# Optimization experiments

Measured on AMD Instinct MI355X. Metric: run time of the kernel, lower is better.

The kernel has to match this reference:

```python
import jax, jax.numpy as jnp
import numpy as np

B, N, E, H = 4, 2048, 288, 8
D = E // H  # head_dim = 36


def setup_inputs() -> dict:
    key = jax.random.key(0)
    ks = jax.random.split(key, 8)
    s = 1.0 / np.sqrt(E)
    return {
        "query": jax.random.normal(ks[0], (B, N, E), jnp.float32),
        "key": jax.random.normal(ks[1], (B, N, E), jnp.float32),
        "value": jax.random.normal(ks[2], (B, N, E), jnp.float32),
        "Wq": jax.random.normal(ks[3], (E, E), jnp.float32) * s,
        "bq": jnp.zeros((E,), jnp.float32),
        "Wk": jax.random.normal(ks[4], (E, E), jnp.float32) * s,
        "bk": jnp.zeros((E,), jnp.float32),
        "Wv": jax.random.normal(ks[5], (E, E), jnp.float32) * s,
        "bv": jnp.zeros((E,), jnp.float32),
        "Wo": jax.random.normal(ks[6], (E, E), jnp.float32) * s,
        "bo": jnp.zeros((E,), jnp.float32),
    }


def reference(query, key, value, Wq, bq, Wk, bk, Wv, bv, Wo, bo):
    scaling = float(D) ** (-0.5)
    q = (query @ Wq + bq) * scaling            # (B, N, E), pre-scaled as in source
    k = key @ Wk + bk                          # (B, N, E)
    v = value @ Wv + bv                        # (B, N, E)
    # split heads: per-head slices along last dim == reshape to (B, N, H, D)
    qh = q.reshape(B, N, H, D)
    kh = k.reshape(B, N, H, D)
    vh = v.reshape(B, N, H, D)
    scores = jnp.einsum("bnhd,bmhd->bhnm", qh, kh)   # (B, H, N, N)
    attn = jax.nn.softmax(scores, axis=-1)
    out = jnp.einsum("bhnm,bmhd->bnhd", attn, vh)    # (B, N, H, D)
    out = out.reshape(B, N, E)                       # concat heads
    return out @ Wo + bo
```

## Files before the change

kernel.cpp:

```cpp
#include <hip/hip_runtime.h>

#define E 288
#define NSEQ 2048
#define BATCH 4
#define NH 8
#define HD 36
#define BH (BATCH * NH)
#define ROWS (BATCH * NSEQ)

typedef _Float16 half8_t __attribute__((ext_vector_type(8)));
typedef _Float16 half4_t __attribute__((ext_vector_type(4)));
typedef float f32x4 __attribute__((ext_vector_type(4)));
typedef int i32x4 __attribute__((ext_vector_type(4)));

__device__ __forceinline__ int sw64(int row, int col) {
  return (row << 6) + ((((col >> 3) ^ row) & 7) << 3) + (col & 7);
}

__device__ __forceinline__ void gld16(const _Float16* g, _Float16* l) {
  __builtin_amdgcn_global_load_lds(
      (const __attribute__((address_space(1))) void*)g,
      (__attribute__((address_space(3))) void*)l, 16, 0, 0);
}

__device__ __forceinline__ float fexp2(float x) {
  return __builtin_amdgcn_exp2f(x);
}

__global__ __launch_bounds__(256) void split_w_kernel(
    const float* __restrict__ Wq, const float* __restrict__ Wk,
    const float* __restrict__ Wv, const float* __restrict__ Wo,
    _Float16* __restrict__ whalf) {
  const int idx = blockIdx.x * 256 + threadIdx.x;
  const int m = idx / (E * E);
  const int rem = idx - m * (E * E);
  const int k = rem / E, n = rem - k * E;
  const float* W = (m == 0) ? Wq : (m == 1) ? Wk : (m == 2) ? Wv : Wo;
  whalf[(size_t)m * (E * E) + n * E + k] = (_Float16)W[rem];
}

#define PM 128
#define PN 96
#define LDA 40

struct QKVArgs {
  const float* x[3];
  const _Float16* w[3];
  const float* bias[3];
  _Float16* out[3];
};

__global__ __launch_bounds__(256, 4) void proj_qkv_kernel(QKVArgs A) {
  __shared__ __align__(16) _Float16 a_h[PM * LDA];
  __shared__ __align__(16) _Float16 w_h[PN * LDA];

  const int tid = threadIdx.x;
  const int lane = tid & 63, wv = tid >> 6;
  const int quad = lane >> 4, l15 = lane & 15;
  const int mode = blockIdx.z;
  const float* __restrict__ x = A.x[mode];
  const _Float16* __restrict__ wh = A.w[mode];
  const int row0 = blockIdx.x * PM, col0 = blockIdx.y * PN;

  f32x4 acc[2][6];
#pragma unroll
  for (int t = 0; t < 2; ++t)
#pragma unroll
    for (int nt = 0; nt < 6; ++nt) acc[t][nt] = (f32x4){0.f, 0.f, 0.f, 0.f};

  float4 apre[4];
  i32x4 wpre[2];
#pragma unroll
  for (int iu = 0; iu < 4; ++iu) {
    const int i = tid + 256 * iu, r = i >> 3, c4 = i & 7;
    apre[iu] = *(const float4*)&x[(size_t)(row0 + r) * E + c4 * 4];
  }
  {
    const int n = tid >> 2, qd = tid & 3;
    wpre[0] = *(const i32x4*)&wh[(size_t)(col0 + n) * E + qd * 8];
    if (tid < 128) {
      const int i = tid + 256, n2 = i >> 2, q2 = i & 3;
      wpre[1] = *(const i32x4*)&wh[(size_t)(col0 + n2) * E + q2 * 8];
    }
  }

  for (int kk = 0; kk < E; kk += 32) {
    __syncthreads();
#pragma unroll
    for (int iu = 0; iu < 4; ++iu) {
      const int i = tid + 256 * iu, r = i >> 3, c4 = i & 7;
      half4_t hv = {(_Float16)apre[iu].x, (_Float16)apre[iu].y,
                    (_Float16)apre[iu].z, (_Float16)apre[iu].w};
      *(half4_t*)&a_h[r * LDA + c4 * 4] = hv;
    }
    {
      const int n = tid >> 2, qd = tid & 3;
      *(i32x4*)&w_h[n * LDA + qd * 8] = wpre[0];
      if (tid < 128) {
        const int i = tid + 256, n2 = i >> 2, q2 = i & 3;
        *(i32x4*)&w_h[n2 * LDA + q2 * 8] = wpre[1];
      }
    }
    if (kk + 32 < E) {
#pragma unroll
      for (int iu = 0; iu < 4; ++iu) {
        const int i = tid + 256 * iu, r = i >> 3, c4 = i & 7;
        apre[iu] = *(const float4*)&x[(size_t)(row0 + r) * E + kk + 32 + c4 * 4];
      }
      const int n = tid >> 2, qd = tid & 3;
      wpre[0] = *(const i32x4*)&wh[(size_t)(col0 + n) * E + kk + 32 + qd * 8];
      if (tid < 128) {
        const int i = tid + 256, n2 = i >> 2, q2 = i & 3;
        wpre[1] = *(const i32x4*)&wh[(size_t)(col0 + n2) * E + kk + 32 + q2 * 8];
      }
    }
    __syncthreads();

    half8_t ah[2];
#pragma unroll
    for (int t = 0; t < 2; ++t)
      ah[t] = *(const half8_t*)&a_h[(wv * 32 + t * 16 + l15) * LDA + quad * 8];
#pragma unroll
    for (int nt = 0; nt < 6; ++nt) {
      const half8_t bh = *(const half8_t*)&w_h[(nt * 16 + l15) * LDA + quad * 8];
#pragma unroll
      for (int t = 0; t < 2; ++t)
        acc[t][nt] = __builtin_amdgcn_mfma_f32_16x16x32_f16(ah[t], bh, acc[t][nt], 0, 0, 0);
    }
  }

  const float* __restrict__ bias = A.bias[mode];
  _Float16* __restrict__ outp = A.out[mode];
  const float scale = (mode == 0) ? 0.24044917348149868f : 1.0f;
#pragma unroll
  for (int nt = 0; nt < 6; ++nt) {
    const int col = col0 + nt * 16 + l15;
    const int h = col / 36, d = col - h * 36;
    const float bc = bias[col];
#pragma unroll
    for (int t = 0; t < 2; ++t) {
#pragma unroll
      for (int r = 0; r < 4; ++r) {
        const int row = row0 + wv * 32 + t * 16 + quad * 4 + r;
        const int b = row >> 11, n = row & (NSEQ - 1);
        const int bh = b * NH + h;
        const _Float16 val = (_Float16)((acc[t][nt][r] + bc) * scale);
        if (mode == 0) {
          outp[((size_t)bh * NSEQ + n) * 64 + d] = val;
        } else {
          const int kt = n >> 6, c = n & 63;
          if (mode == 1) {
            outp[((size_t)bh * 32 + kt) * 4096 + sw64(c, d)] = val;
          } else {
            const int pc = ((c & 15) << 2) | (c >> 4);
            outp[((size_t)bh * 32 + kt) * 3072 + sw64(d, pc)] = val;
          }
        }
      }
    }
  }
}

#define QB 128
#define KT 64
#define SPLIT 4

__device__ __forceinline__ void stage_tile(const _Float16* kg, const _Float16* vg,
                                           _Float16* kb, _Float16* vb, int w,
                                           int lane) {
#pragma unroll
  for (int seg = w; seg < 8; seg += 4)
    gld16(kg + seg * 512 + lane * 8, kb + seg * 512);
  for (int seg = w; seg < 6; seg += 4)
    gld16(vg + seg * 512 + lane * 8, vb + seg * 512);
}

__global__ __launch_bounds__(256, 3) void attn_kernel(
    const _Float16* __restrict__ q16, const _Float16* __restrict__ kblk,
    const _Float16* __restrict__ vblk, float* __restrict__ pacc,
    float* __restrict__ psum) {
  __shared__ __align__(16) _Float16 kbuf[2][KT * 64];
  __shared__ __align__(16) _Float16 vbuf[2][48 * 64];
  __shared__ __align__(16) _Float16 pbuf[QB * 64];

  const int tid = threadIdx.x;
  const int lane = tid & 63;
  const int w = tid >> 6;
  const int quad = lane >> 4;
  const int l15 = lane & 15;

  const int id = blockIdx.x;
  const int xcd = id & 7;
  const int qb = (id >> 3) & 15;
  const int g = id >> 7;
  const int bhc = g * 8 + xcd;
  const int bh = bhc >> 2;
  const int chunk = bhc & 3;
  const int q0 = qb * QB;

  const _Float16* qbase = q16 + ((size_t)bh * NSEQ + q0 + w * 32) * 64;
  half8_t qf[2][2];
#pragma unroll
  for (int t = 0; t < 2; ++t)
#pragma unroll
    for (int kc = 0; kc < 2; ++kc)
      qf[t][kc] = *(const half8_t*)&qbase[(t * 16 + l15) * 64 + kc * 32 + quad * 8];

  f32x4 oacc[2][3];
#pragma unroll
  for (int t = 0; t < 2; ++t)
#pragma unroll
    for (int nt = 0; nt < 3; ++nt) oacc[t][nt] = (f32x4){0.f, 0.f, 0.f, 0.f};
  float ssum[2][4] = {{0.f, 0.f, 0.f, 0.f}, {0.f, 0.f, 0.f, 0.f}};

  const int t0 = chunk * 8;
  const _Float16* kbase = kblk + ((size_t)bh * 32 + t0) * 4096;
  const _Float16* vbase = vblk + ((size_t)bh * 32 + t0) * 3072;

  stage_tile(kbase, vbase, kbuf[0], vbuf[0], w, lane);

  for (int it = 0; it < 8; ++it) {
    const int cur = it & 1;
    __syncthreads();
    if (it + 1 < 8)
      stage_tile(kbase + (it + 1) * 4096, vbase + (it + 1) * 3072,
                 kbuf[cur ^ 1], vbuf[cur ^ 1], w, lane);

#pragma unroll
    for (int t = 0; t < 2; ++t) {
      f32x4 sc[4];
#pragma unroll
      for (int s = 0; s < 4; ++s) {
        const half8_t kf0 = *(const half8_t*)&kbuf[cur][sw64(s * 16 + l15, quad * 8)];
        const half8_t kf1 = *(const half8_t*)&kbuf[cur][sw64(s * 16 + l15, 32 + quad * 8)];
        f32x4 c0 = __builtin_amdgcn_mfma_f32_16x16x32_f16(
            qf[t][0], kf0, (f32x4){0.f, 0.f, 0.f, 0.f}, 0, 0, 0);
        sc[s] = __builtin_amdgcn_mfma_f32_16x16x32_f16(qf[t][1], kf1, c0, 0, 0, 0);
      }
#pragma unroll
      for (int r = 0; r < 4; ++r) {
        const float p0 = fexp2(sc[0][r]);
        const float p1 = fexp2(sc[1][r]);
        const float p2 = fexp2(sc[2][r]);
        const float p3 = fexp2(sc[3][r]);
        ssum[t][r] += (p0 + p1) + (p2 + p3);
        half4_t ph = {(_Float16)p0, (_Float16)p1, (_Float16)p2, (_Float16)p3};
        *(half4_t*)&pbuf[sw64(w * 32 + t * 16 + quad * 4 + r, l15 * 4)] = ph;
      }
    }

#pragma unroll
    for (int kc = 0; kc < 2; ++kc) {
      half8_t vf[3];
#pragma unroll
      for (int nt = 0; nt < 3; ++nt)
        vf[nt] = *(const half8_t*)&vbuf[cur][sw64(nt * 16 + l15, kc * 32 + quad * 8)];
#pragma unroll
      for (int t = 0; t < 2; ++t) {
        const half8_t af = *(const half8_t*)&pbuf[sw64(w * 32 + t * 16 + l15, kc * 32 + quad * 8)];
#pragma unroll
        for (int nt = 0; nt < 3; ++nt)
          oacc[t][nt] = __builtin_amdgcn_mfma_f32_16x16x32_f16(af, vf[nt], oacc[t][nt], 0, 0, 0);
      }
    }
  }

#pragma unroll
  for (int t = 0; t < 2; ++t) {
#pragma unroll
    for (int r = 0; r < 4; ++r) {
      float s = ssum[t][r];
      s += __shfl_xor(s, 1);
      s += __shfl_xor(s, 2);
      s += __shfl_xor(s, 4);
      s += __shfl_xor(s, 8);
      const int row = q0 + w * 32 + t * 16 + quad * 4 + r;
      const size_t gr = (size_t)chunk * (BH * NSEQ) + (size_t)bh * NSEQ + row;
      if (l15 == 0) psum[gr] = s;
#pragma unroll
      for (int nt = 0; nt < 3; ++nt) {
        const int col = nt * 16 + l15;
        if (col < HD) pacc[gr * HD + col] = oacc[t][nt][r];
      }
    }
  }
}

__global__ __launch_bounds__(256) void combine_kernel(
    const float* __restrict__ pacc, const float* __restrict__ psum,
    _Float16* __restrict__ ab_hi, _Float16* __restrict__ ab_lo) {
  const int idx = blockIdx.x * 256 + threadIdx.x;
  if (idx >= BH * NSEQ * HD) return;
  const int gr = idx / HD;
  const int d = idx - gr * HD;

  float a = 0.f, s = 0.f;
#pragma unroll
  for (int c = 0; c < SPLIT; ++c) {
    a += pacc[((size_t)c * (BH * NSEQ) + gr) * HD + d];
    s += psum[(size_t)c * (BH * NSEQ) + gr];
  }
  const float val = a / s;
  const int bh = gr >> 11;
  const int n = gr & (NSEQ - 1);
  const int b = bh >> 3, h = bh & 7;
  const size_t o = ((size_t)(b * NSEQ + n)) * E + h * HD + d;
  const _Float16 hi = (_Float16)val;
  ab_hi[o] = hi;
  ab_lo[o] = (_Float16)(val - (float)hi);
}

__global__ __launch_bounds__(256, 4) void proj_o_kernel(
    const _Float16* __restrict__ xh, const _Float16* __restrict__ xl,
    const _Float16* __restrict__ wh, const float* __restrict__ bias,
    float* __restrict__ out) {
  __shared__ __align__(16) _Float16 a_h[PM * LDA];
  __shared__ __align__(16) _Float16 a_l[PM * LDA];
  __shared__ __align__(16) _Float16 w_h[PN * LDA];

  const int tid = threadIdx.x;
  const int lane = tid & 63, wv = tid >> 6;
  const int quad = lane >> 4, l15 = lane & 15;
  const int row0 = blockIdx.x * PM, col0 = blockIdx.y * PN;

  f32x4 acc[2][6];
#pragma unroll
  for (int t = 0; t < 2; ++t)
#pragma unroll
    for (int nt = 0; nt < 6; ++nt) acc[t][nt] = (f32x4){0.f, 0.f, 0.f, 0.f};

  i32x4 hpre[2], lpre[2], wpre[2];
#pragma unroll
  for (int iu = 0; iu < 2; ++iu) {
    const int i = tid + 256 * iu, r = i >> 2, qd = i & 3;
    hpre[iu] = *(const i32x4*)&xh[(size_t)(row0 + r) * E + qd * 8];
    lpre[iu] = *(const i32x4*)&xl[(size_t)(row0 + r) * E + qd * 8];
  }
  {
    const int n = tid >> 2, qd = tid & 3;
    wpre[0] = *(const i32x4*)&wh[(size_t)(col0 + n) * E + qd * 8];
    if (tid < 128) {
      const int i = tid + 256, n2 = i >> 2, q2 = i & 3;
      wpre[1] = *(const i32x4*)&wh[(size_t)(col0 + n2) * E + q2 * 8];
    }
  }

  for (int kk = 0; kk < E; kk += 32) {
    __syncthreads();
#pragma unroll
    for (int iu = 0; iu < 2; ++iu) {
      const int i = tid + 256 * iu, r = i >> 2, qd = i & 3;
      *(i32x4*)&a_h[r * LDA + qd * 8] = hpre[iu];
      *(i32x4*)&a_l[r * LDA + qd * 8] = lpre[iu];
    }
    {
      const int n = tid >> 2, qd = tid & 3;
      *(i32x4*)&w_h[n * LDA + qd * 8] = wpre[0];
      if (tid < 128) {
        const int i = tid + 256, n2 = i >> 2, q2 = i & 3;
        *(i32x4*)&w_h[n2 * LDA + q2 * 8] = wpre[1];
      }
    }
    if (kk + 32 < E) {
#pragma unroll
      for (int iu = 0; iu < 2; ++iu) {
        const int i = tid + 256 * iu, r = i >> 2, qd = i & 3;
        hpre[iu] = *(const i32x4*)&xh[(size_t)(row0 + r) * E + kk + 32 + qd * 8];
        lpre[iu] = *(const i32x4*)&xl[(size_t)(row0 + r) * E + kk + 32 + qd * 8];
      }
      const int n = tid >> 2, qd = tid & 3;
      wpre[0] = *(const i32x4*)&wh[(size_t)(col0 + n) * E + kk + 32 + qd * 8];
      if (tid < 128) {
        const int i = tid + 256, n2 = i >> 2, q2 = i & 3;
        wpre[1] = *(const i32x4*)&wh[(size_t)(col0 + n2) * E + kk + 32 + q2 * 8];
      }
    }
    __syncthreads();

    half8_t ah[2], al[2];
#pragma unroll
    for (int t = 0; t < 2; ++t) {
      ah[t] = *(const half8_t*)&a_h[(wv * 32 + t * 16 + l15) * LDA + quad * 8];
      al[t] = *(const half8_t*)&a_l[(wv * 32 + t * 16 + l15) * LDA + quad * 8];
    }
#pragma unroll
    for (int nt = 0; nt < 6; ++nt) {
      const half8_t bh = *(const half8_t*)&w_h[(nt * 16 + l15) * LDA + quad * 8];
#pragma unroll
      for (int t = 0; t < 2; ++t) {
        acc[t][nt] = __builtin_amdgcn_mfma_f32_16x16x32_f16(ah[t], bh, acc[t][nt], 0, 0, 0);
        acc[t][nt] = __builtin_amdgcn_mfma_f32_16x16x32_f16(al[t], bh, acc[t][nt], 0, 0, 0);
      }
    }
  }

#pragma unroll
  for (int nt = 0; nt < 6; ++nt) {
    const int col = col0 + nt * 16 + l15;
    const float bc = bias[col];
#pragma unroll
    for (int t = 0; t < 2; ++t) {
#pragma unroll
      for (int r = 0; r < 4; ++r) {
        const int row = row0 + wv * 32 + t * 16 + quad * 4 + r;
        out[(size_t)row * E + col] = acc[t][nt][r] + bc;
      }
    }
  }
}

extern "C" void kernel_launch(void* const* d_in, const int* in_sizes, int n_in,
                              void* d_out, int out_size, void* d_ws,
                              size_t ws_size, hipStream_t stream) {
  const float* query = (const float*)d_in[0];
  const float* key_ = (const float*)d_in[1];
  const float* value = (const float*)d_in[2];
  const float* Wq = (const float*)d_in[3];
  const float* bq = (const float*)d_in[4];
  const float* Wk = (const float*)d_in[5];
  const float* bk = (const float*)d_in[6];
  const float* Wv = (const float*)d_in[7];
  const float* bv = (const float*)d_in[8];
  const float* Wo = (const float*)d_in[9];
  const float* bo = (const float*)d_in[10];
  float* out = (float*)d_out;

  _Float16* q16 = (_Float16*)d_ws;
  _Float16* kblk = q16 + (size_t)BH * NSEQ * 64;
  _Float16* vblk = kblk + (size_t)BH * 32 * 4096;
  float* pacc = (float*)(vblk + (size_t)BH * 32 * 3072);
  float* psum = pacc + (size_t)SPLIT * BH * NSEQ * HD;
  _Float16* whalf = (_Float16*)(psum + (size_t)SPLIT * BH * NSEQ);
  _Float16* ab_hi = whalf + (size_t)4 * E * E;
  _Float16* ab_lo = ab_hi + (size_t)ROWS * E;

  (void)hipMemsetAsync(q16, 0, (size_t)BH * NSEQ * 64 * sizeof(_Float16),
                       stream);

  split_w_kernel<<<(4 * E * E) / 256, 256, 0, stream>>>(Wq, Wk, Wv, Wo, whalf);

  QKVArgs qa;
  qa.x[0] = query; qa.x[1] = key_; qa.x[2] = value;
  qa.w[0] = whalf + 0 * (size_t)(E * E);
  qa.w[1] = whalf + 1 * (size_t)(E * E);
  qa.w[2] = whalf + 2 * (size_t)(E * E);
  qa.bias[0] = bq; qa.bias[1] = bk; qa.bias[2] = bv;
  qa.out[0] = q16; qa.out[1] = kblk; qa.out[2] = vblk;
  proj_qkv_kernel<<<dim3(ROWS / PM, E / PN, 3), 256, 0, stream>>>(qa);

  attn_kernel<<<dim3((NSEQ / QB) * BH * SPLIT), 256, 0, stream>>>(
      q16, kblk, vblk, pacc, psum);

  combine_kernel<<<(BH * NSEQ * HD + 255) / 256, 256, 0, stream>>>(pacc, psum,
                                                                   ab_hi, ab_lo);

  proj_o_kernel<<<dim3(ROWS / PM, E / PN), 256, 0, stream>>>(
      ab_hi, ab_lo, whalf + 3 * (size_t)(E * E), bo, out);
}
```

Baseline: 181.7 us.

## Pre-tile inputs and weights into swizzled fp16 blocks with async LDS loads

A new prep kernel converts the query/key/value activations and all four weights to fp16 in pre-tiled, XOR-swizzled block layouts, and zeroes q16 in the same launch, which replaces the separate memset and weight-split launches. The projection kernels then double-buffer whole tiles straight into LDS with global_load_lds instead of staging through registers and converting in the loop. The attention partial accumulators are stored as fp16, so the combine kernel reads less data and writes vectorised blocked hi/lo outputs. The output projection uses 64-row tiles to get more blocks. In exchange this adds a full extra read and write of the activations in the prep pass, and the fp16 partial sums lose precision.

```diff
diff --git a/kernel.cpp b/kernel.cpp
--- a/kernel.cpp
+++ b/kernel.cpp
@@ -7,6 +7,7 @@
 #define HD 36
 #define BH (BATCH * NH)
 #define ROWS (BATCH * NSEQ)
+#define BHN (BH * NSEQ)
 
 typedef _Float16 half8_t __attribute__((ext_vector_type(8)));
 typedef _Float16 half4_t __attribute__((ext_vector_type(4)));
@@ -17,6 +18,12 @@
   return (row << 6) + ((((col >> 3) ^ row) & 7) << 3) + (col & 7);
 }
 
+__device__ __forceinline__ int toff(int r, int k) {
+  const int rp = r >> 1;
+  const int g = (((r & 1) << 2) + (k >> 3)) ^ (rp & 7);
+  return (rp << 6) + ((g & 7) << 3) + (k & 7);
+}
+
 __device__ __forceinline__ void gld16(const _Float16* g, _Float16* l) {
   __builtin_amdgcn_global_load_lds(
       (const __attribute__((address_space(1))) void*)g,
@@ -27,40 +34,65 @@
   return __builtin_amdgcn_exp2f(x);
 }
 
-__global__ __launch_bounds__(256) void split_w_kernel(
-    const float* __restrict__ Wq, const float* __restrict__ Wk,
-    const float* __restrict__ Wv, const float* __restrict__ Wo,
-    _Float16* __restrict__ whalf) {
-  const int idx = blockIdx.x * 256 + threadIdx.x;
-  const int m = idx / (E * E);
-  const int rem = idx - m * (E * E);
-  const int k = rem / E, n = rem - k * E;
-  const float* W = (m == 0) ? Wq : (m == 1) ? Wk : (m == 2) ? Wv : Wo;
-  whalf[(size_t)m * (E * E) + n * E + k] = (_Float16)W[rem];
+#define XBLK 6912
+#define WBLK 1296
+#define QZBLK 2048
+
+__global__ __launch_bounds__(256) void prep_kernel(
+    const float* __restrict__ xq, const float* __restrict__ xk,
+    const float* __restrict__ xv, const float* __restrict__ Wq,
+    const float* __restrict__ Wk, const float* __restrict__ Wv,
+    const float* __restrict__ Wo, _Float16* __restrict__ x16blk,
+    _Float16* __restrict__ wblk, _Float16* __restrict__ q16) {
+  const int bid = blockIdx.x;
+  const int tid = threadIdx.x;
+  if (bid < XBLK) {
+    const int i = bid * 256 + tid;
+    const int mode = i / (ROWS * 72);
+    const int rem = i - mode * (ROWS * 72);
+    const int row = rem / 72, k4 = rem - row * 72;
+    const float* x = (mode == 0) ? xq : (mode == 1) ? xk : xv;
+    const float4 v = *(const float4*)&x[(size_t)row * E + k4 * 4];
+    half4_t h = {(_Float16)v.x, (_Float16)v.y, (_Float16)v.z, (_Float16)v.w};
+    _Float16* dst = x16blk + (size_t)mode * (64 * 9 * 4096) +
+                    ((((row >> 7) * 9 + (k4 >> 3))) << 12) +
+                    toff(row & 127, (k4 & 7) * 4);
+    *(half4_t*)dst = h;
+  } else if (bid < XBLK + WBLK) {
+    const int j = (bid - XBLK) * 256 + tid;
+    const int m = j / (E * E);
+    const int rem = j - m * (E * E);
+    const int k = rem / E, n = rem - k * E;
+    const float* W = (m == 0) ? Wq : (m == 1) ? Wk : (m == 2) ? Wv : Wo;
+    wblk[(size_t)((m * 3 + n / 96) * 9 + (k >> 5)) * 3072 +
+         toff(n % 96, k & 31)] = (_Float16)W[(size_t)k * E + n];
+  } else {
+    const int j = (bid - XBLK - WBLK) * 256 + tid;
+    ((i32x4*)q16)[j] = (i32x4){0, 0, 0, 0};
+  }
 }
 
 #define PM 128
 #define PN 96
-#define LDA 40
 
 struct QKVArgs {
-  const float* x[3];
-  const _Float16* w[3];
+  const _Float16* x[3];
   const float* bias[3];
   _Float16* out[3];
 };
 
-__global__ __launch_bounds__(256, 4) void proj_qkv_kernel(QKVArgs A) {
-  __shared__ __align__(16) _Float16 a_h[PM * LDA];
-  __shared__ __align__(16) _Float16 w_h[PN * LDA];
+__global__ __launch_bounds__(256, 4) void proj_qkv_kernel(
+    QKVArgs A, const _Float16* __restrict__ wblk) {
+  __shared__ __align__(16) _Float16 abuf[2][4096];
+  __shared__ __align__(16) _Float16 wbuf[2][3072];
 
   const int tid = threadIdx.x;
-  const int lane = tid & 63, wv = tid >> 6;
+  const int lane = tid & 63, w = tid >> 6;
   const int quad = lane >> 4, l15 = lane & 15;
   const int mode = blockIdx.z;
-  const float* __restrict__ x = A.x[mode];
-  const _Float16* __restrict__ wh = A.w[mode];
-  const int row0 = blockIdx.x * PM, col0 = blockIdx.y * PN;
+  const int RB = blockIdx.x, CT = blockIdx.y;
+  const _Float16* __restrict__ ablk = A.x[mode] + (size_t)RB * 9 * 4096;
+  const _Float16* __restrict__ wb = wblk + (size_t)(mode * 3 + CT) * 9 * 3072;
 
   f32x4 acc[2][6];
 #pragma unroll
@@ -68,70 +100,41 @@
 #pragma unroll
     for (int nt = 0; nt < 6; ++nt) acc[t][nt] = (f32x4){0.f, 0.f, 0.f, 0.f};
 
-  float4 apre[4];
-  i32x4 wpre[2];
-#pragma unroll
-  for (int iu = 0; iu < 4; ++iu) {
-    const int i = tid + 256 * iu, r = i >> 3, c4 = i & 7;
-    apre[iu] = *(const float4*)&x[(size_t)(row0 + r) * E + c4 * 4];
-  }
-  {
-    const int n = tid >> 2, qd = tid & 3;
-    wpre[0] = *(const i32x4*)&wh[(size_t)(col0 + n) * E + qd * 8];
-    if (tid < 128) {
-      const int i = tid + 256, n2 = i >> 2, q2 = i & 3;
-      wpre[1] = *(const i32x4*)&wh[(size_t)(col0 + n2) * E + q2 * 8];
-    }
-  }
-
-  for (int kk = 0; kk < E; kk += 32) {
+#pragma unroll
+  for (int seg = w; seg < 8; seg += 4)
+    gld16(ablk + seg * 512 + lane * 8, abuf[0] + seg * 512);
+  for (int seg = w; seg < 6; seg += 4)
+    gld16(wb + seg * 512 + lane * 8, wbuf[0] + seg * 512);
+
+  for (int C = 0; C < 9; ++C) {
+    const int cur = C & 1;
     __syncthreads();
-#pragma unroll
-    for (int iu = 0; iu < 4; ++iu) {
-      const int i = tid + 256 * iu, r = i >> 3, c4 = i & 7;
-      half4_t hv = {(_Float16)apre[iu].x, (_Float16)apre[iu].y,
-                    (_Float16)apre[iu].z, (_Float16)apre[iu].w};
-      *(half4_t*)&a_h[r * LDA + c4 * 4] = hv;
-    }
-    {
-      const int n = tid >> 2, qd = tid & 3;
-      *(i32x4*)&w_h[n * LDA + qd * 8] = wpre[0];
-      if (tid < 128) {
-        const int i = tid + 256, n2 = i >> 2, q2 = i & 3;
-        *(i32x4*)&w_h[n2 * LDA + q2 * 8] = wpre[1];
-      }
-    }
-    if (kk + 32 < E) {
-#pragma unroll
-      for (int iu = 0; iu < 4; ++iu) {
-        const int i = tid + 256 * iu, r = i >> 3, c4 = i & 7;
-        apre[iu] = *(const float4*)&x[(size_t)(row0 + r) * E + kk + 32 + c4 * 4];
-      }
-      const int n = tid >> 2, qd = tid & 3;
-      wpre[0] = *(const i32x4*)&wh[(size_t)(col0 + n) * E + kk + 32 + qd * 8];
-      if (tid < 128) {
-        const int i = tid + 256, n2 = i >> 2, q2 = i & 3;
-        wpre[1] = *(const i32x4*)&wh[(size_t)(col0 + n2) * E + kk + 32 + q2 * 8];
-      }
-    }
-    __syncthreads();
-
+    if (C + 1 < 9) {
+#pragma unroll
+      for (int seg = w; seg < 8; seg += 4)
+        gld16(ablk + (C + 1) * 4096 + seg * 512 + lane * 8,
+              abuf[cur ^ 1] + seg * 512);
+      for (int seg = w; seg < 6; seg += 4)
+        gld16(wb + (C + 1) * 3072 + seg * 512 + lane * 8,
+              wbuf[cur ^ 1] + seg * 512);
+    }
     half8_t ah[2];
 #pragma unroll
     for (int t = 0; t < 2; ++t)
-      ah[t] = *(const half8_t*)&a_h[(wv * 32 + t * 16 + l15) * LDA + quad * 8];
+      ah[t] = *(const half8_t*)&abuf[cur][toff(w * 32 + t * 16 + l15, quad * 8)];
 #pragma unroll
     for (int nt = 0; nt < 6; ++nt) {
-      const half8_t bh = *(const half8_t*)&w_h[(nt * 16 + l15) * LDA + quad * 8];
+      const half8_t bf = *(const half8_t*)&wbuf[cur][toff(nt * 16 + l15, quad * 8)];
 #pragma unroll
       for (int t = 0; t < 2; ++t)
-        acc[t][nt] = __builtin_amdgcn_mfma_f32_16x16x32_f16(ah[t], bh, acc[t][nt], 0, 0, 0);
+        acc[t][nt] = __builtin_amdgcn_mfma_f32_16x16x32_f16(ah[t], bf, acc[t][nt], 0, 0, 0);
     }
   }
 
   const float* __restrict__ bias = A.bias[mode];
   _Float16* __restrict__ outp = A.out[mode];
   const float scale = (mode == 0) ? 0.24044917348149868f : 1.0f;
+  const int row0 = RB * PM, col0 = CT * PN;
 #pragma unroll
   for (int nt = 0; nt < 6; ++nt) {
     const int col = col0 + nt * 16 + l15;
@@ -141,7 +144,7 @@
     for (int t = 0; t < 2; ++t) {
 #pragma unroll
       for (int r = 0; r < 4; ++r) {
-        const int row = row0 + wv * 32 + t * 16 + quad * 4 + r;
+        const int row = row0 + w * 32 + t * 16 + quad * 4 + r;
         const int b = row >> 11, n = row & (NSEQ - 1);
         const int bh = b * NH + h;
         const _Float16 val = (_Float16)((acc[t][nt][r] + bc) * scale);
@@ -177,7 +180,7 @@
 
 __global__ __launch_bounds__(256, 3) void attn_kernel(
     const _Float16* __restrict__ q16, const _Float16* __restrict__ kblk,
-    const _Float16* __restrict__ vblk, float* __restrict__ pacc,
+    const _Float16* __restrict__ vblk, _Float16* __restrict__ pacc16,
     float* __restrict__ psum) {
   __shared__ __align__(16) _Float16 kbuf[2][KT * 64];
   __shared__ __align__(16) _Float16 vbuf[2][48 * 64];
@@ -275,136 +278,106 @@
       s += __shfl_xor(s, 4);
       s += __shfl_xor(s, 8);
       const int row = q0 + w * 32 + t * 16 + quad * 4 + r;
-      const size_t gr = (size_t)chunk * (BH * NSEQ) + (size_t)bh * NSEQ + row;
+      const size_t gr = (size_t)chunk * BHN + (size_t)bh * NSEQ + row;
       if (l15 == 0) psum[gr] = s;
 #pragma unroll
       for (int nt = 0; nt < 3; ++nt) {
         const int col = nt * 16 + l15;
-        if (col < HD) pacc[gr * HD + col] = oacc[t][nt][r];
+        if (col < HD) pacc16[gr * HD + col] = (_Float16)oacc[t][nt][r];
       }
     }
   }
 }
 
 __global__ __launch_bounds__(256) void combine_kernel(
-    const float* __restrict__ pacc, const float* __restrict__ psum,
-    _Float16* __restrict__ ab_hi, _Float16* __restrict__ ab_lo) {
+    const _Float16* __restrict__ pacc16, const float* __restrict__ psum,
+    _Float16* __restrict__ abh, _Float16* __restrict__ abl) {
   const int idx = blockIdx.x * 256 + threadIdx.x;
-  if (idx >= BH * NSEQ * HD) return;
-  const int gr = idx / HD;
-  const int d = idx - gr * HD;
-
-  float a = 0.f, s = 0.f;
+  if (idx >= BHN * 9) return;
+  const int gr = idx / 9;
+  const int d4 = idx - gr * 9;
+
+  float a[4] = {0.f, 0.f, 0.f, 0.f};
+  float s = 0.f;
 #pragma unroll
   for (int c = 0; c < SPLIT; ++c) {
-    a += pacc[((size_t)c * (BH * NSEQ) + gr) * HD + d];
-    s += psum[(size_t)c * (BH * NSEQ) + gr];
-  }
-  const float val = a / s;
+    const half4_t p = *(const half4_t*)&pacc16[((size_t)c * BHN + gr) * HD + d4 * 4];
+#pragma unroll
+    for (int j = 0; j < 4; ++j) a[j] += (float)p[j];
+    s += psum[(size_t)c * BHN + gr];
+  }
+  const float inv = 1.0f / s;
   const int bh = gr >> 11;
   const int n = gr & (NSEQ - 1);
   const int b = bh >> 3, h = bh & 7;
-  const size_t o = ((size_t)(b * NSEQ + n)) * E + h * HD + d;
-  const _Float16 hi = (_Float16)val;
-  ab_hi[o] = hi;
-  ab_lo[o] = (_Float16)(val - (float)hi);
+  const int row = b * NSEQ + n;
+  const int col = h * 36 + d4 * 4;
+
+  half4_t hv, lv;
+#pragma unroll
+  for (int j = 0; j < 4; ++j) {
+    const float val = a[j] * inv;
+    const _Float16 hi = (_Float16)val;
+    hv[j] = hi;
+    lv[j] = (_Float16)(val - (float)hi);
+  }
+  const size_t o = (size_t)((row >> 6) * 9 + (col >> 5)) * 2048 + toff(row & 63, col & 31);
+  *(half4_t*)&abh[o] = hv;
+  *(half4_t*)&abl[o] = lv;
 }
 
 __global__ __launch_bounds__(256, 4) void proj_o_kernel(
-    const _Float16* __restrict__ xh, const _Float16* __restrict__ xl,
-    const _Float16* __restrict__ wh, const float* __restrict__ bias,
+    const _Float16* __restrict__ abh, const _Float16* __restrict__ abl,
+    const _Float16* __restrict__ wblk_o, const float* __restrict__ bias,
     float* __restrict__ out) {
-  __shared__ __align__(16) _Float16 a_h[PM * LDA];
-  __shared__ __align__(16) _Float16 a_l[PM * LDA];
-  __shared__ __align__(16) _Float16 w_h[PN * LDA];
+  __shared__ __align__(16) _Float16 hbuf[2][2048];
+  __shared__ __align__(16) _Float16 lbuf[2][2048];
+  __shared__ __align__(16) _Float16 wbuf[2][3072];
 
   const int tid = threadIdx.x;
-  const int lane = tid & 63, wv = tid >> 6;
+  const int lane = tid & 63, w = tid >> 6;
   const int quad = lane >> 4, l15 = lane & 15;
-  const int row0 = blockIdx.x * PM, col0 = blockIdx.y * PN;
-
-  f32x4 acc[2][6];
-#pragma unroll
-  for (int t = 0; t < 2; ++t)
-#pragma unroll
-    for (int nt = 0; nt < 6; ++nt) acc[t][nt] = (f32x4){0.f, 0.f, 0.f, 0.f};
-
-  i32x4 hpre[2], lpre[2], wpre[2];
-#pragma unroll
-  for (int iu = 0; iu < 2; ++iu) {
-    const int i = tid + 256 * iu, r = i >> 2, qd = i & 3;
-    hpre[iu] = *(const i32x4*)&xh[(size_t)(row0 + r) * E + qd * 8];
-    lpre[iu] = *(const i32x4*)&xl[(size_t)(row0 + r) * E + qd * 8];
-  }
-  {
-    const int n = tid >> 2, qd = tid & 3;
-    wpre[0] = *(const i32x4*)&wh[(size_t)(col0 + n) * E + qd * 8];
-    if (tid < 128) {
-      const int i = tid + 256, n2 = i >> 2, q2 = i & 3;
-      wpre[1] = *(const i32x4*)&wh[(size_t)(col0 + n2) * E + q2 * 8];
-    }
-  }
-
-  for (int kk = 0; kk < E; kk += 32) {
+  const int RB = blockIdx.x, CT = blockIdx.y;
+  const _Float16* __restrict__ hblk = abh + (size_t)RB * 9 * 2048;
+  const _Float16* __restrict__ lblk = abl + (size_t)RB * 9 * 2048;
+  const _Float16* __restrict__ wb = wblk_o + (size_t)CT * 9 * 3072;
+
+  f32x4 acc[6];
+#pragma unroll
+  for (int nt = 0; nt < 6; ++nt) acc[nt] = (f32x4){0.f, 0.f, 0.f, 0.f};
+
+  gld16(hblk + w * 512 + lane * 8, hbuf[0] + w * 512);
+  gld16(lblk + w * 512 + lane * 8, lbuf[0] + w * 512);
+  for (int seg = w; seg < 6; seg += 4)
+    gld16(wb + seg * 512 + lane * 8, wbuf[0] + seg * 512);
+
+  for (int C = 0; C < 9; ++C) {
+    const int cur = C & 1;
     __syncthreads();
-#pragma unroll
-    for (int iu = 0; iu < 2; ++iu) {
-      const int i = tid + 256 * iu, r = i >> 2, qd = i & 3;
-      *(i32x4*)&a_h[r * LDA + qd * 8] = hpre[iu];
-      *(i32x4*)&a_l[r * LDA + qd * 8] = lpre[iu];
-    }
-    {
-      const int n = tid >> 2, qd = tid & 3;
-      *(i32x4*)&w_h[n * LDA + qd * 8] = wpre[0];
-      if (tid < 128) {
-        const int i = tid + 256, n2 = i >> 2, q2 = i & 3;
-        *(i32x4*)&w_h[n2 * LDA + q2 * 8] = wpre[1];
-      }
-    }
-    if (kk + 32 < E) {
-#pragma unroll
-      for (int iu = 0; iu < 2; ++iu) {
-        const int i = tid + 256 * iu, r = i >> 2, qd = i & 3;
-        hpre[iu] = *(const i32x4*)&xh[(size_t)(row0 + r) * E + kk + 32 + qd * 8];
-        lpre[iu] = *(const i32x4*)&xl[(size_t)(row0 + r) * E + kk + 32 + qd * 8];
-      }
-      const int n = tid >> 2, qd = tid & 3;
-      wpre[0] = *(const i32x4*)&wh[(size_t)(col0 + n) * E + kk + 32 + qd * 8];
-      if (tid < 128) {
-        const int i = tid + 256, n2 = i >> 2, q2 = i & 3;
-        wpre[1] = *(const i32x4*)&wh[(size_t)(col0 + n2) * E + kk + 32 + q2 * 8];
-      }
-    }
-    __syncthreads();
-
-    half8_t ah[2], al[2];
-#pragma unroll
-    for (int t = 0; t < 2; ++t) {
-      ah[t] = *(const half8_t*)&a_h[(wv * 32 + t * 16 + l15) * LDA + quad * 8];
-      al[t] = *(const half8_t*)&a_l[(wv * 32 + t * 16 + l15) * LDA + quad * 8];
-    }
+    if (C + 1 < 9) {
+      gld16(hblk + (C + 1) * 2048 + w * 512 + lane * 8, hbuf[cur ^ 1] + w * 512);
+      gld16(lblk + (C + 1) * 2048 + w * 512 + lane * 8, lbuf[cur ^ 1] + w * 512);
+      for (int seg = w; seg < 6; seg += 4)
+        gld16(wb + (C + 1) * 3072 + seg * 512 + lane * 8, wbuf[cur ^ 1] + seg * 512);
+    }
+    const half8_t ah = *(const half8_t*)&hbuf[cur][toff(w * 16 + l15, quad * 8)];
+    const half8_t al = *(const half8_t*)&lbuf[cur][toff(w * 16 + l15, quad * 8)];
 #pragma unroll
     for (int nt = 0; nt < 6; ++nt) {
-      const half8_t bh = *(const half8_t*)&w_h[(nt * 16 + l15) * LDA + quad * 8];
-#pragma unroll
-      for (int t = 0; t < 2; ++t) {
-        acc[t][nt] = __builtin_amdgcn_mfma_f32_16x16x32_f16(ah[t], bh, acc[t][nt], 0, 0, 0);
-        acc[t][nt] = __builtin_amdgcn_mfma_f32_16x16x32_f16(al[t], bh, acc[t][nt], 0, 0, 0);
-      }
+      const half8_t bf = *(const half8_t*)&wbuf[cur][toff(nt * 16 + l15, quad * 8)];
+      acc[nt] = __builtin_amdgcn_mfma_f32_16x16x32_f16(ah, bf, acc[nt], 0, 0, 0);
+      acc[nt] = __builtin_amdgcn_mfma_f32_16x16x32_f16(al, bf, acc[nt], 0, 0, 0);
     }
   }
 
 #pragma unroll
   for (int nt = 0; nt < 6; ++nt) {
-    const int col = col0 + nt * 16 + l15;
+    const int col = CT * PN + nt * 16 + l15;
     const float bc = bias[col];
 #pragma unroll
-    for (int t = 0; t < 2; ++t) {
-#pragma unroll
-      for (int r = 0; r < 4; ++r) {
-        const int row = row0 + wv * 32 + t * 16 + quad * 4 + r;
-        out[(size_t)row * E + col] = acc[t][nt][r] + bc;
-      }
+    for (int r = 0; r < 4; ++r) {
+      const int row = RB * 64 + w * 16 + quad * 4 + r;
+      out[(size_t)row * E + col] = acc[nt][r] + bc;
     }
   }
 }
@@ -428,32 +401,29 @@
   _Float16* q16 = (_Float16*)d_ws;
   _Float16* kblk = q16 + (size_t)BH * NSEQ * 64;
   _Float16* vblk = kblk + (size_t)BH * 32 * 4096;
-  float* pacc = (float*)(vblk + (size_t)BH * 32 * 3072);
-  float* psum = pacc + (size_t)SPLIT * BH * NSEQ * HD;
-  _Float16* whalf = (_Float16*)(psum + (size_t)SPLIT * BH * NSEQ);
-  _Float16* ab_hi = whalf + (size_t)4 * E * E;
-  _Float16* ab_lo = ab_hi + (size_t)ROWS * E;
-
-  (void)hipMemsetAsync(q16, 0, (size_t)BH * NSEQ * 64 * sizeof(_Float16),
-                       stream);
-
-  split_w_kernel<<<(4 * E * E) / 256, 256, 0, stream>>>(Wq, Wk, Wv, Wo, whalf);
+  _Float16* x16blk = vblk + (size_t)BH * 32 * 3072;
+  _Float16* wblk = x16blk + (size_t)3 * 64 * 9 * 4096;
+  _Float16* abh = wblk + (size_t)4 * 3 * 9 * 3072;
+  _Float16* abl = abh + (size_t)128 * 9 * 2048;
+  _Float16* pacc16 = abl + (size_t)128 * 9 * 2048;
+  float* psum = (float*)(pacc16 + (size_t)SPLIT * BHN * HD);
+
+  prep_kernel<<<XBLK + WBLK + QZBLK, 256, 0, stream>>>(
+      query, key_, value, Wq, Wk, Wv, Wo, x16blk, wblk, q16);
 
   QKVArgs qa;
-  qa.x[0] = query; qa.x[1] = key_; qa.x[2] = value;
-  qa.w[0] = whalf + 0 * (size_t)(E * E);
-  qa.w[1] = whalf + 1 * (size_t)(E * E);
-  qa.w[2] = whalf + 2 * (size_t)(E * E);
+  qa.x[0] = x16blk + 0 * (size_t)(64 * 9 * 4096);
+  qa.x[1] = x16blk + 1 * (size_t)(64 * 9 * 4096);
+  qa.x[2] = x16blk + 2 * (size_t)(64 * 9 * 4096);
   qa.bias[0] = bq; qa.bias[1] = bk; qa.bias[2] = bv;
   qa.out[0] = q16; qa.out[1] = kblk; qa.out[2] = vblk;
-  proj_qkv_kernel<<<dim3(ROWS / PM, E / PN, 3), 256, 0, stream>>>(qa);
+  proj_qkv_kernel<<<dim3(ROWS / PM, E / PN, 3), 256, 0, stream>>>(qa, wblk);
 
   attn_kernel<<<dim3((NSEQ / QB) * BH * SPLIT), 256, 0, stream>>>(
-      q16, kblk, vblk, pacc, psum);
-
-  combine_kernel<<<(BH * NSEQ * HD + 255) / 256, 256, 0, stream>>>(pacc, psum,
-                                                                   ab_hi, ab_lo);
-
-  proj_o_kernel<<<dim3(ROWS / PM, E / PN), 256, 0, stream>>>(
-      ab_hi, ab_lo, whalf + 3 * (size_t)(E * E), bo, out);
-}
+      q16, kblk, vblk, pacc16, psum);
+
+  combine_kernel<<<(BHN * 9) / 256, 256, 0, stream>>>(pacc16, psum, abh, abl);
+
+  proj_o_kernel<<<dim3(ROWS / 64, E / PN), 256, 0, stream>>>(
+      abh, abl, wblk + (size_t)3 * 3 * 9 * 3072, bo, out);
+}
```

Measured after the change: 172.8 us. 1.05x faster.
